# Kernel optimization log

Hardware: AMD Instinct MI355X
Metric: run time of the kernel (lower is better)

The kernel has to match this reference:

```python
import jax, jax.numpy as jnp
import numpy as np

B, S, H = 2, 512, 1024
D = 24            # hdim_proj_dim
MLP_H = 96        # hdim_mlp_hidden
VAL_IN = 2 * H    # concat_only
OUT_HID = 2 * max(128, H // 2)  # 1024


def setup_inputs() -> dict:
    key = jax.random.key(0)
    ks = jax.random.split(key, 12)
    sc = 0.02
    return {
        "H_j": jax.random.normal(ks[0], (B, S, H), jnp.float32),
        "H_i": jax.random.normal(ks[1], (B, S, H), jnp.float32),
        "attn_mask": jnp.ones((B, S), jnp.float32),
        "p_j": jax.random.normal(ks[2], (H, D), jnp.float32) * sc,
        "p_i": jax.random.normal(ks[3], (H, D), jnp.float32) * sc,
        "W1": jax.random.normal(ks[4], (4 * D, MLP_H), jnp.float32) * sc,
        "b1": jnp.zeros((MLP_H,), jnp.float32),
        "W2": jax.random.normal(ks[5], (MLP_H, 1), jnp.float32) * sc,
        "b2": jnp.zeros((1,), jnp.float32),
        "Wv1": jax.random.normal(ks[6], (VAL_IN, OUT_HID), jnp.float32) * sc,
        "bv1": jnp.zeros((OUT_HID,), jnp.float32),
        "Wv2": jax.random.normal(ks[7], (OUT_HID, H), jnp.float32) * sc,
        "bv2": jnp.zeros((H,), jnp.float32),
        "alpha": jnp.asarray(0.05, jnp.float32),
    }


def reference(H_j, H_i, attn_mask, p_j, p_i, W1, b1, W2, b2, Wv1, bv1, Wv2, bv2, alpha):
    # Low-dim projections: [B,S,D]
    Zj = jnp.einsum('bsh,hd->bsd', H_j, p_j)
    Zi = jnp.einsum('bsh,hd->bsd', H_i, p_i)
    # 4-term pairwise features: [B,S,S,4D]
    Zj_b = jnp.broadcast_to(Zj[:, :, None, :], (B, S, S, D))
    Zi_b = jnp.broadcast_to(Zi[:, None, :, :], (B, S, S, D))
    pair = jnp.concatenate([Zj_b, Zi_b, Zj_b * Zi_b, jnp.abs(Zj_b - Zi_b)], axis=-1)
    # Pair-score MLP -> logits [B,S,S]
    h = jax.nn.relu(jnp.einsum('bjif,fm->bjim', pair, W1) + b1)
    logits = (jnp.einsum('bjim,mo->bjio', h, W2) + b2)[..., 0]
    # additive key-side mask (same as torch _expand_mask_last)
    logits = logits + (1.0 - attn_mask)[:, None, :] * jnp.finfo(logits.dtype).min
    # token_temp == 1.0 -> no scaling
    probs = jax.nn.softmax(logits, axis=-1)  # over keys i
    ctx = jnp.einsum('bji,bih->bjh', probs, H_i)  # [B,S,H]
    # Value fusion MLP (concat_only), dropout is identity in eval
    msg_in = jnp.concatenate([ctx, H_j], axis=-1)  # [B,S,2H]
    msg = jax.nn.relu(jnp.einsum('bsf,fo->bso', msg_in, Wv1) + bv1)
    msg = jnp.einsum('bso,oh->bsh', msg, Wv2) + bv2
    return alpha * msg
```

## Files before the change

### kernel.cpp

```cpp
#include <hip/hip_runtime.h>
#include <math.h>

#define B_    2
#define S_    512
#define HDIM  1024
#define D_    24
#define M_    96
#define ROWS  (B_*S_)

typedef _Float16 half8 __attribute__((ext_vector_type(8)));
typedef float    f32x4 __attribute__((ext_vector_type(4)));
typedef unsigned short ushort8 __attribute__((ext_vector_type(8)));

__device__ __forceinline__ void transpose_tile64_cache(
    const float* __restrict__ in, _Float16* __restrict__ out,
    int R, int C, int xt, int yt, int t) {
  int R0 = yt * 64, C0 = xt * 64;
  int c = t >> 2, rq = (t & 3) * 16;
  _Float16 o[16];
  const float* src = in + (size_t)(R0 + rq) * C + C0 + c;
#pragma unroll
  for (int e = 0; e < 16; ++e) o[e] = (_Float16)src[(size_t)e * C];
  _Float16* dst = out + (size_t)(C0 + c) * R + R0 + rq;
  *(ushort8*)dst = *(ushort8*)o;
  *(ushort8*)(dst + 8) = *(ushort8*)&o[8];
}

__device__ __forceinline__ void proj_mfma64(
    const float* __restrict__ H, const float* __restrict__ P,
    float* __restrict__ Z, _Float16* __restrict__ Himg,
    int r0, char* smem, int t) {
  const int w = t >> 6, l = t & 63;
  const int lo = l & 15, hi = l >> 4;
  const int row = r0 + w * 16 + lo;
  const float* hrow = H + (size_t)row * HDIM;
  f32x4 acc0 = {}, acc1 = {};

  for (int ph = 0; ph < 2; ++ph) {
    if (ph) __syncthreads();
    for (int q = 0; q < 8; ++q) {
      int s = t + q * 256;
      int slo = s & 15, shi = (s >> 4) & 3, snt = (s >> 6) & 1, sst = s >> 7;
      int d = snt * 16 + slo;
      half8 v = {};
      if (d < D_) {
        int k = (ph * 16 + sst) * 32 + shi * 8;
#pragma unroll
        for (int e = 0; e < 8; ++e)
          v[e] = (_Float16)P[(size_t)(k + e) * D_ + d];
      }
      *(half8*)(smem + s * 16) = v;
    }
    __syncthreads();

    for (int st = 0; st < 16; ++st) {
      int step = ph * 16 + st;
      const float* src = hrow + step * 32 + hi * 8;
      float4 v0 = *(const float4*)src;
      float4 v1 = *(const float4*)(src + 4);
      half8 a8;
      a8[0] = (_Float16)v0.x; a8[1] = (_Float16)v0.y;
      a8[2] = (_Float16)v0.z; a8[3] = (_Float16)v0.w;
      a8[4] = (_Float16)v1.x; a8[5] = (_Float16)v1.y;
      a8[6] = (_Float16)v1.z; a8[7] = (_Float16)v1.w;
      *(half8*)(Himg + (size_t)row * HDIM + step * 32 + hi * 8) = a8;
      half8 b0 = *(const half8*)(smem + ((st * 2 + 0) * 64 + l) * 16);
      half8 b1 = *(const half8*)(smem + ((st * 2 + 1) * 64 + l) * 16);
      acc0 = __builtin_amdgcn_mfma_f32_16x16x32_f16(a8, b0, acc0, 0, 0, 0);
      acc1 = __builtin_amdgcn_mfma_f32_16x16x32_f16(a8, b1, acc1, 0, 0, 0);
    }
  }
#pragma unroll
  for (int rg = 0; rg < 4; ++rg) {
    int zr = r0 + w * 16 + hi * 4 + rg;
    Z[(size_t)zr * D_ + lo] = acc0[rg];
    if (lo < 8) Z[(size_t)zr * D_ + 16 + lo] = acc1[rg];
  }
}

__global__ __launch_bounds__(256) void prep_kernel(
    const float* __restrict__ Hj, const float* __restrict__ Hi,
    const float* __restrict__ pj, const float* __restrict__ pi,
    const float* __restrict__ W1, const float* __restrict__ Wv1,
    const float* __restrict__ Wv2,
    _Float16* __restrict__ HjH, _Float16* __restrict__ HiH,
    _Float16* __restrict__ Wv1aT, _Float16* __restrict__ Wv1bT,
    _Float16* __restrict__ Wv2T, _Float16* __restrict__ Wimg,
    float* __restrict__ Zj, float* __restrict__ Zi) {
  __shared__ __attribute__((aligned(16))) char smem[32768];
  const int bid = blockIdx.x;
  const int t = threadIdx.x;

  if (bid < 16) {
    proj_mfma64(Hj, pj, Zj, HjH, bid * 64, smem, t);
  } else if (bid < 32) {
    proj_mfma64(Hi, pi, Zi, HiH, (bid - 16) * 64, smem, t);
  } else if (bid < 36) {
    int c = (bid - 32) * 256 + t;
    half8 v = {};
    if (c < 864) {
      int kc = c / 96, m = c - kc * 96;
#pragma unroll
      for (int e = 0; e < 8; ++e)
        v[e] = (_Float16)W1[(24 + kc * 8 + e) * M_ + m];
    }
    *(half8*)(Wimg + (size_t)c * 8) = v;
  } else if (bid < 292) {
    int id = bid - 36;
    transpose_tile64_cache(Wv1, Wv1aT, HDIM, HDIM, id & 15, id >> 4, t);
  } else if (bid < 548) {
    int id = bid - 292;
    transpose_tile64_cache(Wv1 + (size_t)HDIM * HDIM, Wv1bT, HDIM, HDIM,
                           id & 15, id >> 4, t);
  } else {
    int id = bid - 548;
    transpose_tile64_cache(Wv2, Wv2T, HDIM, HDIM, id & 15, id >> 4, t);
  }
}

#define FOFFB   0
#define LOGOFFB 40960
#define ZJOFFB  (LOGOFFB + 2048)
#define W2OFFB  (ZJOFFB + 96)
#define AJOFFB  (W2OFFB + 384)
#define REDOFFB (AJOFFB + 384)
#define ZCOFFB  (REDOFFB + 32)
#define LDSB    (ZCOFFB + 16)

__global__ __launch_bounds__(256, 3) void pair_gt_kernel(
    const float* __restrict__ Zj, const float* __restrict__ Zi,
    const float* __restrict__ W1, const float* __restrict__ b1,
    const float* __restrict__ W2, const _Float16* __restrict__ Wimg,
    const float* __restrict__ mask, _Float16* __restrict__ probs,
    const _Float16* __restrict__ Wv1aT, const _Float16* __restrict__ HiH,
    _Float16* __restrict__ GT) {
  __shared__ __attribute__((aligned(16))) char smem[LDSB];
  const int t = threadIdx.x;
  const int w = t >> 6, l = t & 63;
  const int lo = l & 15, hi = l >> 4;

  if (blockIdx.x < 256) {
    int id = blockIdx.x;
    int zb = id >> 7, rem = id & 127;
    int n0 = (rem & 7) * 64, m0 = (rem >> 3) * 64;
    const _Float16* Bb = HiH + (size_t)zb * S_ * HDIM;
    _Float16* GTb = GT + (size_t)zb * HDIM * S_;

    const int sr = (w << 4) + (l >> 2);
    const int sk = ((l & 3) ^ ((l >> 3) & 3)) << 3;
    const int mq = w >> 1, nq = w & 1;
    int offA[2], offB[2];
#pragma unroll
    for (int i = 0; i < 2; ++i) {
      int ra = mq * 32 + i * 16 + (l & 15);
      offA[i] = ra * 64 + (((l >> 4) ^ ((ra >> 1) & 3)) << 4);
      int rb = nq * 32 + i * 16 + (l & 15);
      offB[i] = 4096 + rb * 64 + (((l >> 4) ^ ((rb >> 1) & 3)) << 4);
    }
    f32x4 acc[2][2] = {};

    auto stage = [&](int tt) {
      char* buf = smem + (tt & 3) * 8192;
      int kg = (tt << 5) + sk;
      const _Float16* ga = Wv1aT + (size_t)(m0 + sr) * HDIM + kg;
      __builtin_amdgcn_global_load_lds(
          (const __attribute__((address_space(1))) void*)ga,
          (__attribute__((address_space(3))) void*)(buf + (w << 10)), 16, 0, 0);
      const _Float16* gb = Bb + (size_t)(n0 + sr) * HDIM + kg;
      __builtin_amdgcn_global_load_lds(
          (const __attribute__((address_space(1))) void*)gb,
          (__attribute__((address_space(3))) void*)(buf + 4096 + (w << 10)), 16, 0, 0);
    };
    stage(0); stage(1); stage(2);
    const int NT = HDIM >> 5;
    for (int tt = 0; tt < NT; ++tt) {
      if (tt + 2 < NT)      asm volatile("s_waitcnt vmcnt(4)" ::: "memory");
      else if (tt + 1 < NT) asm volatile("s_waitcnt vmcnt(2)" ::: "memory");
      else                  asm volatile("s_waitcnt vmcnt(0)" ::: "memory");
      __builtin_amdgcn_s_barrier();
      __builtin_amdgcn_sched_barrier(0);
      const char* buf = smem + (tt & 3) * 8192;
      half8 a0 = *(const half8*)(buf + offA[0]);
      half8 a1 = *(const half8*)(buf + offA[1]);
      half8 b0 = *(const half8*)(buf + offB[0]);
      half8 b1v = *(const half8*)(buf + offB[1]);
      acc[0][0] = __builtin_amdgcn_mfma_f32_16x16x32_f16(a0, b0, acc[0][0], 0, 0, 0);
      acc[0][1] = __builtin_amdgcn_mfma_f32_16x16x32_f16(a0, b1v, acc[0][1], 0, 0, 0);
      acc[1][0] = __builtin_amdgcn_mfma_f32_16x16x32_f16(a1, b0, acc[1][0], 0, 0, 0);
      acc[1][1] = __builtin_amdgcn_mfma_f32_16x16x32_f16(a1, b1v, acc[1][1], 0, 0, 0);
      if (tt + 3 < NT) stage(tt + 3);
    }
    const int lr = l & 15, lq = l >> 4;
#pragma unroll
    for (int mi = 0; mi < 2; ++mi)
#pragma unroll
      for (int ni = 0; ni < 2; ++ni) {
        int col = n0 + nq * 32 + ni * 16 + lr;
#pragma unroll
        for (int rg = 0; rg < 4; ++rg) {
          int row = m0 + mq * 32 + mi * 16 + lq * 4 + rg;
          GTb[(size_t)row * S_ + col] = (_Float16)acc[mi][ni][rg];
        }
      }
    return;
  }

  const int rj = blockIdx.x - 256;
  const int b = rj >> 9;
  float* zjL    = (float*)(smem + ZJOFFB);
  float* W2s    = (float*)(smem + W2OFFB);
  float* ajL    = (float*)(smem + AJOFFB);
  float* logits = (float*)(smem + LOGOFFB);
  float* red    = (float*)(smem + REDOFFB);

  if (t < D_) zjL[t] = Zj[(size_t)rj * D_ + t];
  if (t < M_) {
    W2s[t] = W2[t];
    float aj = b1[t];
#pragma unroll
    for (int d = 0; d < D_; ++d)
      aj = fmaf(Zj[(size_t)rj * D_ + d], W1[d * M_ + t], aj);
    ajL[t] = aj;
  }
  if (t == 0) {
    half8 z = {};
    *(half8*)(smem + ZCOFFB) = z;
  }

  half8 wf[6][3];
#pragma unroll
  for (int mh = 0; mh < 6; ++mh)
#pragma unroll
    for (int ks = 0; ks < 3; ++ks) {
      int kc = ks * 4 + hi;
      half8 v = {};
      if (kc < 10)
        v = *(const half8*)(Wimg + (size_t)(kc * 96 + mh * 16 + lo) * 8);
      wf[mh][ks] = v;
    }

  __syncthreads();

  if (hi == 1) {
#pragma unroll
    for (int mh = 0; mh < 6; ++mh)
      wf[mh][2][0] = (_Float16)ajL[mh * 16 + lo];
  }
  float w2r[6][4];
#pragma unroll
  for (int mh = 0; mh < 6; ++mh)
#pragma unroll
    for (int r = 0; r < 4; ++r) w2r[mh][r] = W2s[mh * 16 + hi * 4 + r];

  for (int p = 0; p < 2; ++p) {
    {
      int i = p * 256 + t;
      const float* zi = Zi + (size_t)(b * S_ + i) * D_;
      float ziv[D_];
#pragma unroll
      for (int q = 0; q < 6; ++q) {
        float4 v = ((const float4*)zi)[q];
        ziv[q * 4 + 0] = v.x; ziv[q * 4 + 1] = v.y;
        ziv[q * 4 + 2] = v.z; ziv[q * 4 + 3] = v.w;
      }
#pragma unroll
      for (int kc = 0; kc < 3; ++kc) {
        half8 v;
#pragma unroll
        for (int e = 0; e < 8; ++e) v[e] = (_Float16)ziv[kc * 8 + e];
        *(half8*)(smem + FOFFB + (kc * 256 + t) * 16) = v;
      }
#pragma unroll
      for (int kc = 0; kc < 3; ++kc) {
        half8 v;
#pragma unroll
        for (int e = 0; e < 8; ++e) {
          int d = kc * 8 + e;
          v[e] = (_Float16)(zjL[d] * ziv[d]);
        }
        *(half8*)(smem + FOFFB + ((kc + 3) * 256 + t) * 16) = v;
      }
#pragma unroll
      for (int kc = 0; kc < 3; ++kc) {
        half8 v;
#pragma unroll
        for (int e = 0; e < 8; ++e) {
          int d = kc * 8 + e;
          v[e] = (_Float16)fabsf(zjL[d] - ziv[d]);
        }
        *(half8*)(smem + FOFFB + ((kc + 6) * 256 + t) * 16) = v;
      }
      if (p == 0) {
        half8 v = {};
        v[0] = (_Float16)1.0f;
        *(half8*)(smem + FOFFB + (9 * 256 + t) * 16) = v;
      }
    }
    __syncthreads();

#pragma unroll
    for (int nt = 0; nt < 4; ++nt) {
      half8 ff[3];
#pragma unroll
      for (int ks = 0; ks < 3; ++ks) {
        int kc = ks * 4 + hi;
        int off = (kc < 10) ? (FOFFB + (kc * 256 + w * 64 + nt * 16 + lo) * 16) : ZCOFFB;
        ff[ks] = *(const half8*)(smem + off);
      }
      f32x4 a6[6] = {};
      __builtin_amdgcn_s_setprio(1);
#pragma unroll
      for (int ks = 0; ks < 3; ++ks)
#pragma unroll
        for (int mh = 0; mh < 6; ++mh)
          a6[mh] = __builtin_amdgcn_mfma_f32_16x16x32_f16(wf[mh][ks], ff[ks], a6[mh], 0, 0, 0);
      __builtin_amdgcn_s_setprio(0);
      float part = 0.f;
#pragma unroll
      for (int mh = 0; mh < 6; ++mh)
#pragma unroll
        for (int r = 0; r < 4; ++r)
          part = fmaf(fmaxf(a6[mh][r], 0.f), w2r[mh][r], part);
      part += __shfl_xor(part, 16);
      part += __shfl_xor(part, 32);
      if (hi == 0) logits[p * 256 + w * 64 + nt * 16 + lo] = part;
    }
    __syncthreads();
  }

  float m1 = mask[b * S_ + t], m2 = mask[b * S_ + t + 256];
  float lg1 = logits[t]       + (1.0f - m1) * (-3.40282347e38f);
  float lg2 = logits[t + 256] + (1.0f - m2) * (-3.40282347e38f);
  float mx = fmaxf(lg1, lg2);
#pragma unroll
  for (int off = 32; off > 0; off >>= 1) mx = fmaxf(mx, __shfl_xor(mx, off));
  if (l == 0) red[w] = mx;
  __syncthreads();
  float rmax = fmaxf(fmaxf(red[0], red[1]), fmaxf(red[2], red[3]));
  float e1 = __expf(lg1 - rmax);
  float e2 = __expf(lg2 - rmax);
  float s = e1 + e2;
#pragma unroll
  for (int off = 32; off > 0; off >>= 1) s += __shfl_xor(s, off);
  if (l == 0) red[4 + w] = s;
  __syncthreads();
  float inv = 1.0f / (red[4] + red[5] + red[6] + red[7]);
  probs[(size_t)rj * S_ + t]       = (_Float16)(e1 * inv);
  probs[(size_t)rj * S_ + t + 256] = (_Float16)(e2 * inv);
}

template <bool SWZ, bool HASA1, bool HASB1, bool RELU, bool FINAL, bool OUTH>
__global__ __launch_bounds__(512) void mfma_gemm_kernel(
    const _Float16* __restrict__ A0, const _Float16* __restrict__ A1,
    const _Float16* __restrict__ B0, const _Float16* __restrict__ B1,
    const float* __restrict__ bias, const float* __restrict__ alpha_ptr,
    void* __restrict__ Cout, int M, int N, int K0, int K1,
    long aB0, long aB1, long bB0, long cB) {
  __shared__ __attribute__((aligned(16))) char smem[65536];
  const int t = threadIdx.x;
  const int w = t >> 6, l = t & 63;
  const int g = w >> 2, wq = w & 3;
  const int K = K0 + K1;
  const int KH = K >> 1;
  const int NT = KH >> 5;
  int n0, m0, zb;
  if (SWZ) {
    int s = (blockIdx.x & 7) * 32 + (blockIdx.x >> 3);
    n0 = (s & 15) * 64; m0 = (s >> 4) * 64; zb = 0;
  } else {
    n0 = blockIdx.x * 64; m0 = blockIdx.y * 64; zb = blockIdx.z;
  }
  const _Float16* A0b = A0 + (size_t)zb * aB0;
  const _Float16* A1b = HASA1 ? (A1 + (size_t)zb * aB1) : nullptr;
  const _Float16* B0b = B0 + (size_t)zb * bB0;
  const int ldB0 = HASB1 ? K0 : K;
  char* gls = smem + (g << 15);

  const int sr = (wq << 4) + (l >> 2);
  const int sk = ((l & 3) ^ ((l >> 3) & 3)) << 3;

  const int mq = wq >> 1, nq = wq & 1;
  int offA[2], offB[2];
#pragma unroll
  for (int i = 0; i < 2; ++i) {
    int ra = mq * 32 + i * 16 + (l & 15);
    offA[i] = ra * 64 + (((l >> 4) ^ ((ra >> 1) & 3)) << 4);
    int rb = nq * 32 + i * 16 + (l & 15);
    offB[i] = 4096 + rb * 64 + (((l >> 4) ^ ((rb >> 1) & 3)) << 4);
  }

  f32x4 acc[2][2] = {};

  auto stage = [&](int tt) {
    char* buf = gls + (tt & 3) * 8192;
    int kg = g * KH + (tt << 5) + sk;
    const _Float16* ga;
    if (HASA1 && kg >= K0) ga = A1b + (size_t)(m0 + sr) * K1 + (kg - K0);
    else                   ga = A0b + (size_t)(m0 + sr) * K0 + kg;
    __builtin_amdgcn_global_load_lds(
        (const __attribute__((address_space(1))) void*)ga,
        (__attribute__((address_space(3))) void*)(buf + (wq << 10)), 16, 0, 0);
    const _Float16* gb;
    if (HASB1 && kg >= K0) gb = B1 + (size_t)(n0 + sr) * K1 + (kg - K0);
    else                   gb = B0b + (size_t)(n0 + sr) * ldB0 + kg;
    __builtin_amdgcn_global_load_lds(
        (const __attribute__((address_space(1))) void*)gb,
        (__attribute__((address_space(3))) void*)(buf + 4096 + (wq << 10)), 16, 0, 0);
  };

  stage(0);
  stage(1);
  stage(2);

  for (int tt = 0; tt < NT; ++tt) {
    if (tt + 2 < NT)      asm volatile("s_waitcnt vmcnt(4)" ::: "memory");
    else if (tt + 1 < NT) asm volatile("s_waitcnt vmcnt(2)" ::: "memory");
    else                  asm volatile("s_waitcnt vmcnt(0)" ::: "memory");
    __builtin_amdgcn_s_barrier();
    __builtin_amdgcn_sched_barrier(0);
    const char* buf = gls + (tt & 3) * 8192;
    half8 a0 = *(const half8*)(buf + offA[0]);
    half8 a1 = *(const half8*)(buf + offA[1]);
    half8 b0 = *(const half8*)(buf + offB[0]);
    half8 b1v = *(const half8*)(buf + offB[1]);
    acc[0][0] = __builtin_amdgcn_mfma_f32_16x16x32_f16(a0, b0, acc[0][0], 0, 0, 0);
    acc[0][1] = __builtin_amdgcn_mfma_f32_16x16x32_f16(a0, b1v, acc[0][1], 0, 0, 0);
    acc[1][0] = __builtin_amdgcn_mfma_f32_16x16x32_f16(a1, b0, acc[1][0], 0, 0, 0);
    acc[1][1] = __builtin_amdgcn_mfma_f32_16x16x32_f16(a1, b1v, acc[1][1], 0, 0, 0);
    if (tt + 3 < NT) stage(tt + 3);
  }

  const int lr = l & 15, lq = l >> 4;
  float* redm = (float*)smem;
  __syncthreads();
  if (g == 1) {
#pragma unroll
    for (int mi = 0; mi < 2; ++mi)
#pragma unroll
      for (int ni = 0; ni < 2; ++ni)
#pragma unroll
        for (int rg = 0; rg < 4; ++rg)
          redm[(mq * 32 + mi * 16 + lq * 4 + rg) * 68 + nq * 32 + ni * 16 + lr] =
              acc[mi][ni][rg];
  }
  __syncthreads();
  if (g == 0) {
    const float alpha = FINAL ? *alpha_ptr : 1.0f;
    const size_t cbase = (size_t)zb * cB;
#pragma unroll
    for (int mi = 0; mi < 2; ++mi)
#pragma unroll
      for (int ni = 0; ni < 2; ++ni) {
        int col = n0 + nq * 32 + ni * 16 + lr;
        float bv = bias ? bias[col] : 0.0f;
#pragma unroll
        for (int rg = 0; rg < 4; ++rg) {
          int row = m0 + mq * 32 + mi * 16 + lq * 4 + rg;
          float x = acc[mi][ni][rg] +
                    redm[(mq * 32 + mi * 16 + lq * 4 + rg) * 68 + nq * 32 + ni * 16 + lr] +
                    bv;
          if (RELU) x = fmaxf(x, 0.f);
          if (FINAL) x *= alpha;
          if (OUTH)
            ((_Float16*)Cout)[cbase + (size_t)row * N + col] = (_Float16)x;
          else
            ((float*)Cout)[cbase + (size_t)row * N + col] = x;
        }
      }
  }
}

extern "C" void kernel_launch(void* const* d_in, const int* in_sizes, int n_in,
                              void* d_out, int out_size, void* d_ws, size_t ws_size,
                              hipStream_t stream) {
  const float* Hj   = (const float*)d_in[0];
  const float* Hi   = (const float*)d_in[1];
  const float* mask = (const float*)d_in[2];
  const float* pj   = (const float*)d_in[3];
  const float* pi   = (const float*)d_in[4];
  const float* W1   = (const float*)d_in[5];
  const float* b1   = (const float*)d_in[6];
  const float* W2   = (const float*)d_in[7];
  const float* Wv1  = (const float*)d_in[9];
  const float* bv1  = (const float*)d_in[10];
  const float* Wv2  = (const float*)d_in[11];
  const float* bv2  = (const float*)d_in[12];
  const float* alpha = (const float*)d_in[13];

  char* w = (char*)d_ws;
  float* Zj  = (float*)w;            w += (size_t)ROWS * D_ * 4;
  float* Zi  = (float*)w;            w += (size_t)ROWS * D_ * 4;
  _Float16* Wimg   = (_Float16*)w;   w += (size_t)1024 * 16;
  _Float16* probsH = (_Float16*)w;   w += (size_t)B_ * S_ * S_ * 2;
  _Float16* HjH    = (_Float16*)w;   w += (size_t)ROWS * HDIM * 2;
  _Float16* HiH    = (_Float16*)w;   w += (size_t)ROWS * HDIM * 2;
  _Float16* Wv1aT  = (_Float16*)w;   w += (size_t)HDIM * HDIM * 2;
  _Float16* Wv1bT  = (_Float16*)w;   w += (size_t)HDIM * HDIM * 2;
  _Float16* Wv2T   = (_Float16*)w;   w += (size_t)HDIM * HDIM * 2;
  _Float16* GT     = (_Float16*)w;   w += (size_t)B_ * HDIM * S_ * 2;
  _Float16* hidH   = (_Float16*)w;   w += (size_t)ROWS * HDIM * 2;
  float* out = (float*)d_out;

  prep_kernel<<<804, 256, 0, stream>>>(Hj, Hi, pj, pi, W1, Wv1, Wv2,
                                       HjH, HiH, Wv1aT, Wv1bT, Wv2T, Wimg,
                                       Zj, Zi);

  pair_gt_kernel<<<ROWS + 256, 256, 0, stream>>>(Zj, Zi, W1, b1, W2, Wimg,
                                                 mask, probsH, Wv1aT, HiH, GT);

  mfma_gemm_kernel<false, true, true, true, false, true>
      <<<dim3(16, 8, 2), 512, 0, stream>>>(
      probsH, HjH, GT, Wv1bT, bv1, nullptr, hidH,
      S_, HDIM, S_, HDIM,
      (long)S_ * S_, (long)S_ * HDIM, (long)HDIM * S_, (long)S_ * HDIM);

  mfma_gemm_kernel<true, false, false, false, true, false>
      <<<dim3(256), 512, 0, stream>>>(
      hidH, nullptr, Wv2T, nullptr, bv2, alpha, out,
      ROWS, HDIM, HDIM, 0, 0, 0, 0, 0);
}
```

Baseline: 66.23 us.

## Precompute Zi·W1 key-side bias in prep and shrink pair MLP K dimension

```diff
diff --git a/kernel.cpp b/kernel.cpp
--- a/kernel.cpp
+++ b/kernel.cpp
@@ -26,10 +26,12 @@
   *(ushort8*)(dst + 8) = *(ushort8*)&o[8];
 }
 
+template <bool DOBI>
 __device__ __forceinline__ void proj_mfma64(
     const float* __restrict__ H, const float* __restrict__ P,
+    const float* __restrict__ W1,
     float* __restrict__ Z, _Float16* __restrict__ Himg,
-    int r0, char* smem, int t) {
+    float* __restrict__ Bi, int r0, char* smem, int t) {
   const int w = t >> 6, l = t & 63;
   const int lo = l & 15, hi = l >> 4;
   const int row = r0 + w * 16 + lo;
@@ -76,6 +78,34 @@
     Z[(size_t)zr * D_ + lo] = acc0[rg];
     if (lo < 8) Z[(size_t)zr * D_ + 16 + lo] = acc1[rg];
   }
+
+  if (DOBI) {
+    __syncthreads();
+    _Float16* ldsZ = (_Float16*)smem;
+#pragma unroll
+    for (int rg = 0; rg < 4; ++rg) {
+      int rr = w * 16 + hi * 4 + rg;
+      ldsZ[rr * 32 + lo] = (_Float16)acc0[rg];
+      ldsZ[rr * 32 + 16 + lo] = (lo < 8) ? (_Float16)acc1[rg] : (_Float16)0.0f;
+    }
+    __syncthreads();
+    half8 a8 = *(const half8*)(&ldsZ[(w * 16 + lo) * 32 + hi * 8]);
+#pragma unroll
+    for (int n6 = 0; n6 < 6; ++n6) {
+      half8 b8;
+#pragma unroll
+      for (int e = 0; e < 8; ++e) {
+        int d = hi * 8 + e;
+        b8[e] = (d < D_) ? (_Float16)W1[(D_ + d) * M_ + n6 * 16 + lo]
+                         : (_Float16)0.0f;
+      }
+      f32x4 accB = {};
+      accB = __builtin_amdgcn_mfma_f32_16x16x32_f16(a8, b8, accB, 0, 0, 0);
+#pragma unroll
+      for (int rg = 0; rg < 4; ++rg)
+        Bi[(size_t)(r0 + w * 16 + hi * 4 + rg) * M_ + n6 * 16 + lo] = accB[rg];
+    }
+  }
 }
 
 __global__ __launch_bounds__(256) void prep_kernel(
@@ -86,23 +116,24 @@
     _Float16* __restrict__ HjH, _Float16* __restrict__ HiH,
     _Float16* __restrict__ Wv1aT, _Float16* __restrict__ Wv1bT,
     _Float16* __restrict__ Wv2T, _Float16* __restrict__ Wimg,
-    float* __restrict__ Zj, float* __restrict__ Zi) {
+    float* __restrict__ Zj, float* __restrict__ Zi,
+    float* __restrict__ BiF) {
   __shared__ __attribute__((aligned(16))) char smem[32768];
   const int bid = blockIdx.x;
   const int t = threadIdx.x;
 
   if (bid < 16) {
-    proj_mfma64(Hj, pj, Zj, HjH, bid * 64, smem, t);
+    proj_mfma64<false>(Hj, pj, W1, Zj, HjH, nullptr, bid * 64, smem, t);
   } else if (bid < 32) {
-    proj_mfma64(Hi, pi, Zi, HiH, (bid - 16) * 64, smem, t);
+    proj_mfma64<true>(Hi, pi, W1, Zi, HiH, BiF, (bid - 16) * 64, smem, t);
   } else if (bid < 36) {
     int c = (bid - 32) * 256 + t;
     half8 v = {};
-    if (c < 864) {
+    if (c < 576) {
       int kc = c / 96, m = c - kc * 96;
 #pragma unroll
       for (int e = 0; e < 8; ++e)
-        v[e] = (_Float16)W1[(24 + kc * 8 + e) * M_ + m];
+        v[e] = (_Float16)W1[(48 + kc * 8 + e) * M_ + m];
     }
     *(half8*)(Wimg + (size_t)c * 8) = v;
   } else if (bid < 292) {
@@ -119,13 +150,13 @@
 }
 
 #define FOFFB   0
-#define LOGOFFB 40960
+#define LOGOFFB 24576
 #define ZJOFFB  (LOGOFFB + 2048)
 #define W2OFFB  (ZJOFFB + 96)
 #define AJOFFB  (W2OFFB + 384)
 #define REDOFFB (AJOFFB + 384)
 #define ZCOFFB  (REDOFFB + 32)
-#define LDSB    (ZCOFFB + 16)
+#define LDSB    32768
 
 __global__ __launch_bounds__(256, 3) void pair_gt_kernel(
     const float* __restrict__ Zj, const float* __restrict__ Zi,
@@ -133,7 +164,7 @@
     const float* __restrict__ W2, const _Float16* __restrict__ Wimg,
     const float* __restrict__ mask, _Float16* __restrict__ probs,
     const _Float16* __restrict__ Wv1aT, const _Float16* __restrict__ HiH,
-    _Float16* __restrict__ GT) {
+    _Float16* __restrict__ GT, const float* __restrict__ BiF) {
   __shared__ __attribute__((aligned(16))) char smem[LDSB];
   const int t = threadIdx.x;
   const int w = t >> 6, l = t & 63;
@@ -227,30 +258,28 @@
     *(half8*)(smem + ZCOFFB) = z;
   }
 
-  half8 wf[6][3];
+  half8 wf[6][2];
 #pragma unroll
   for (int mh = 0; mh < 6; ++mh)
 #pragma unroll
-    for (int ks = 0; ks < 3; ++ks) {
+    for (int ks = 0; ks < 2; ++ks) {
       int kc = ks * 4 + hi;
       half8 v = {};
-      if (kc < 10)
+      if (kc < 6)
         v = *(const half8*)(Wimg + (size_t)(kc * 96 + mh * 16 + lo) * 8);
       wf[mh][ks] = v;
     }
 
   __syncthreads();
 
-  if (hi == 1) {
-#pragma unroll
-    for (int mh = 0; mh < 6; ++mh)
-      wf[mh][2][0] = (_Float16)ajL[mh * 16 + lo];
-  }
-  float w2r[6][4];
+  float w2r[6][4], ajr[6][4];
 #pragma unroll
   for (int mh = 0; mh < 6; ++mh)
 #pragma unroll
-    for (int r = 0; r < 4; ++r) w2r[mh][r] = W2s[mh * 16 + hi * 4 + r];
+    for (int r = 0; r < 4; ++r) {
+      w2r[mh][r] = W2s[mh * 16 + hi * 4 + r];
+      ajr[mh][r] = ajL[mh * 16 + hi * 4 + r];
+    }
 
   for (int p = 0; p < 2; ++p) {
     {
@@ -267,18 +296,11 @@
       for (int kc = 0; kc < 3; ++kc) {
         half8 v;
 #pragma unroll
-        for (int e = 0; e < 8; ++e) v[e] = (_Float16)ziv[kc * 8 + e];
-        *(half8*)(smem + FOFFB + (kc * 256 + t) * 16) = v;
-      }
-#pragma unroll
-      for (int kc = 0; kc < 3; ++kc) {
-        half8 v;
-#pragma unroll
         for (int e = 0; e < 8; ++e) {
           int d = kc * 8 + e;
           v[e] = (_Float16)(zjL[d] * ziv[d]);
         }
-        *(half8*)(smem + FOFFB + ((kc + 3) * 256 + t) * 16) = v;
+        *(half8*)(smem + FOFFB + (kc * 256 + t) * 16) = v;
       }
 #pragma unroll
       for (int kc = 0; kc < 3; ++kc) {
@@ -288,29 +310,31 @@
           int d = kc * 8 + e;
           v[e] = (_Float16)fabsf(zjL[d] - ziv[d]);
         }
-        *(half8*)(smem + FOFFB + ((kc + 6) * 256 + t) * 16) = v;
-      }
-      if (p == 0) {
-        half8 v = {};
-        v[0] = (_Float16)1.0f;
-        *(half8*)(smem + FOFFB + (9 * 256 + t) * 16) = v;
+        *(half8*)(smem + FOFFB + ((kc + 3) * 256 + t) * 16) = v;
       }
     }
     __syncthreads();
 
 #pragma unroll
     for (int nt = 0; nt < 4; ++nt) {
-      half8 ff[3];
-#pragma unroll
-      for (int ks = 0; ks < 3; ++ks) {
+      int i = p * 256 + w * 64 + nt * 16 + lo;
+      half8 ff[2];
+#pragma unroll
+      for (int ks = 0; ks < 2; ++ks) {
         int kc = ks * 4 + hi;
-        int off = (kc < 10) ? (FOFFB + (kc * 256 + w * 64 + nt * 16 + lo) * 16) : ZCOFFB;
+        int off = (kc < 6) ? (FOFFB + (kc * 256 + w * 64 + nt * 16 + lo) * 16) : ZCOFFB;
         ff[ks] = *(const half8*)(smem + off);
       }
-      f32x4 a6[6] = {};
+      f32x4 a6[6];
+#pragma unroll
+      for (int mh = 0; mh < 6; ++mh) {
+        f32x4 bi4 = *(const f32x4*)(BiF + (size_t)(b * S_ + i) * M_ + mh * 16 + hi * 4);
+#pragma unroll
+        for (int r = 0; r < 4; ++r) a6[mh][r] = bi4[r] + ajr[mh][r];
+      }
       __builtin_amdgcn_s_setprio(1);
 #pragma unroll
-      for (int ks = 0; ks < 3; ++ks)
+      for (int ks = 0; ks < 2; ++ks)
 #pragma unroll
         for (int mh = 0; mh < 6; ++mh)
           a6[mh] = __builtin_amdgcn_mfma_f32_16x16x32_f16(wf[mh][ks], ff[ks], a6[mh], 0, 0, 0);
@@ -490,6 +514,7 @@
   char* w = (char*)d_ws;
   float* Zj  = (float*)w;            w += (size_t)ROWS * D_ * 4;
   float* Zi  = (float*)w;            w += (size_t)ROWS * D_ * 4;
+  float* BiF = (float*)w;            w += (size_t)ROWS * M_ * 4;
   _Float16* Wimg   = (_Float16*)w;   w += (size_t)1024 * 16;
   _Float16* probsH = (_Float16*)w;   w += (size_t)B_ * S_ * S_ * 2;
   _Float16* HjH    = (_Float16*)w;   w += (size_t)ROWS * HDIM * 2;
@@ -503,10 +528,11 @@
 
   prep_kernel<<<804, 256, 0, stream>>>(Hj, Hi, pj, pi, W1, Wv1, Wv2,
                                        HjH, HiH, Wv1aT, Wv1bT, Wv2T, Wimg,
-                                       Zj, Zi);
+                                       Zj, Zi, BiF);
 
   pair_gt_kernel<<<ROWS + 256, 256, 0, stream>>>(Zj, Zi, W1, b1, W2, Wimg,
-                                                 mask, probsH, Wv1aT, HiH, GT);
+                                                 mask, probsH, Wv1aT, HiH, GT,
+                                                 BiF);
 
   mfma_gemm_kernel<false, true, true, true, false, true>
       <<<dim3(16, 8, 2), 512, 0, stream>>>(
```

After: 89.28 us. 1.35x slower.
